# Performance work log

Hardware: AMD Instinct MI355X
Metric: run time of the kernel (lower is better)

## Reference

```python
import jax, jax.numpy as jnp
import numpy as np

N = 262144
H = 256
R = 32


def setup_inputs() -> dict:
    key = jax.random.key(0)
    ks = jax.random.split(key, 16)
    s = 1.0 / np.sqrt(H)
    return {
        "x": jax.random.normal(ks[0], (N, 1), jnp.float32),
        "t": jax.random.uniform(ks[1], (N, 1), jnp.float32),
        "start_w": jax.random.normal(ks[2], (H, 2), jnp.float32) * 0.5,
        "start_b": jax.random.normal(ks[3], (H,), jnp.float32) * 0.1,
        "end_w": jax.random.normal(ks[4], (1, H), jnp.float32) * s,
        "end_b": jax.random.normal(ks[5], (1,), jnp.float32) * 0.1,
        "col_0": jax.random.normal(ks[6], (H, R), jnp.float32) * s,
        "col_1": jax.random.normal(ks[7], (H, R), jnp.float32) * s,
        "col_2": jax.random.normal(ks[8], (H, R), jnp.float32) * s,
        "row_0": jax.random.normal(ks[9], (H, R), jnp.float32) * s,
        "row_1": jax.random.normal(ks[10], (H, R), jnp.float32) * s,
        "row_2": jax.random.normal(ks[11], (H, R), jnp.float32) * s,
        "alpha_0": jax.random.normal(ks[12], (R,), jnp.float32),
        "alpha_1": jax.random.normal(ks[13], (R,), jnp.float32),
        "alpha_2": jax.random.normal(ks[14], (R,), jnp.float32),
    }


def reference(x, t, start_w, start_b, end_w, end_b,
              col_0, col_1, col_2, row_0, row_1, row_2,
              alpha_0, alpha_1, alpha_2):
    # inputs: [N,2] -> start Linear -> tanh
    inp = jnp.concatenate([x, t], axis=1)
    h = jnp.tanh(inp @ start_w.T + start_b)  # [N, H]
    # three low-rank blocks: h @ (col * diag(alpha)) @ row.T, then tanh.
    # col_basis @ diag(alpha) == col_basis * alpha[None, :] (column scaling)
    for col, row, alpha in ((col_0, row_0, alpha_0),
                            (col_1, row_1, alpha_1),
                            (col_2, row_2, alpha_2)):
        h = jnp.tanh((h @ (col * alpha)) @ row.T)  # [N,H]->[N,R]->[N,H]
    return h @ end_w.T + end_b  # [N, 1]
```

## Files before the change

### kernel.cpp

```cpp
#include <hip/hip_runtime.h>


typedef _Float16 half4_t __attribute__((ext_vector_type(4)));
typedef __fp16   fp16x2  __attribute__((ext_vector_type(2)));
typedef float    float4_t __attribute__((ext_vector_type(4)));

#define TANH_SCALE 2.885390081777927f
#define MFMA16 __builtin_amdgcn_mfma_f32_16x16x16f16

namespace {

struct alignas(16) Smem {
  half4_t ctf[3 * 16 * 2 * 64];
  half4_t rwf[3 * 16 * 2 * 64];
  float w0[256], w1[256], bb[256];
  float ew[256];
  float rsC[3 * 32];
};

__device__ __forceinline__ half4_t pack4(float4_t v) {
  union { fp16x2 f2[2]; half4_t h4; } u;
  u.f2[0] = __builtin_amdgcn_cvt_pkrtz(v.x, v.y);
  u.f2[1] = __builtin_amdgcn_cvt_pkrtz(v.z, v.w);
  return u.h4;
}

__device__ __forceinline__ float inv_pre(float y) {
  return __builtin_amdgcn_rcpf(__builtin_amdgcn_exp2f(y) + 1.0f);
}

__device__ __forceinline__ half4_t inv4(float4_t v) {
  float4_t r;
  r.x = inv_pre(v.x); r.y = inv_pre(v.y);
  r.z = inv_pre(v.z); r.w = inv_pre(v.w);
  return pack4(r);
}

__global__ __launch_bounds__(1024)
__attribute__((amdgpu_waves_per_eu(4, 4)))
void pinn_fused(
    const float* __restrict__ xg, const float* __restrict__ tg,
    const float* __restrict__ sw, const float* __restrict__ sb,
    const float* __restrict__ ewp, const float* __restrict__ ebp,
    const float* __restrict__ c0, const float* __restrict__ c1,
    const float* __restrict__ c2, const float* __restrict__ r0,
    const float* __restrict__ r1, const float* __restrict__ r2,
    const float* __restrict__ a0, const float* __restrict__ a1,
    const float* __restrict__ a2, float* __restrict__ out, int n)
{
  __shared__ Smem sm;
  const int tid = threadIdx.x;

  for (int e = tid; e < 3 * 16 * 2 * 64; e += 1024) {
    const int lane_ = e & 63;
    const int sel   = (e >> 6) & 1;
    const int t_    = (e >> 7) & 15;
    const int k_    = e >> 11;
    const int m_ = lane_ & 15, q_ = lane_ >> 4;
    const float* ck = (k_ == 0) ? c0 : (k_ == 1) ? c1 : c2;
    const float* rk = (k_ == 0) ? r0 : (k_ == 1) ? r1 : r2;
    const float* ak = (k_ == 0) ? a0 : (k_ == 1) ? a1 : a2;
    {
      const int r = sel * 16 + m_;
      const float av = ak[r] * -2.0f;
      const int j0 = 16 * t_ + 4 * q_;
      half4_t v;
      v.x = (_Float16)(ck[(j0 + 0) * 32 + r] * av);
      v.y = (_Float16)(ck[(j0 + 1) * 32 + r] * av);
      v.z = (_Float16)(ck[(j0 + 2) * 32 + r] * av);
      v.w = (_Float16)(ck[(j0 + 3) * 32 + r] * av);
      sm.ctf[e] = v;
    }
    {
      const int j = 16 * t_ + m_;
      const int rr = sel * 16 + 4 * q_;
      half4_t v;
      v.x = (_Float16)(rk[j * 32 + rr + 0] * TANH_SCALE);
      v.y = (_Float16)(rk[j * 32 + rr + 1] * TANH_SCALE);
      v.z = (_Float16)(rk[j * 32 + rr + 2] * TANH_SCALE);
      v.w = (_Float16)(rk[j * 32 + rr + 3] * TANH_SCALE);
      sm.rwf[e] = v;
    }
  }
  if (tid < 256) {
    sm.w0[tid] = sw[2 * tid] * TANH_SCALE;
    sm.w1[tid] = sw[2 * tid + 1] * TANH_SCALE;
    sm.bb[tid] = sb[tid] * TANH_SCALE;
    sm.ew[tid] = ewp[tid] * -2.0f;
  }
  __syncthreads();

  if (tid < 96) {
    const int k_ = tid >> 5, r = tid & 31;
    const int sel = r >> 4, mm = r & 15;
    float s = 0.0f;
    for (int t = 0; t < 16; ++t)
      for (int qq = 0; qq < 4; ++qq) {
        const half4_t v = sm.ctf[((k_ * 16 + t) * 2 + sel) * 64 + 16 * qq + mm];
        s += (float)v.x + (float)v.y + (float)v.z + (float)v.w;
      }
    sm.rsC[k_ * 32 + r] = -0.5f * s;
  }
  __syncthreads();

  const int wave = tid >> 6;
  const int lane = tid & 63;
  const int m = lane & 15;
  const int q = lane >> 4;
  const int wo = 4 * q;
  const float ebv = ebp[0];
  const int tiles = n >> 4;

  float ewsum = 0.0f;
  for (int t = 0; t < 16; ++t) {
    const float4_t e4 = *(const float4_t*)&sm.ew[t * 16 + wo];
    ewsum += e4.x + e4.y + e4.z + e4.w;
  }
  ewsum *= -0.5f;

  const float4_t z4 = {0.f, 0.f, 0.f, 0.f};

#pragma unroll 1
  for (int g = (blockIdx.x * 16 + wave) * 4; g < tiles; g += 16384) {
    float xm[4], tm[4];
#pragma unroll
    for (int s = 0; s < 4; ++s) {
      xm[s] = xg[(g + s) * 16 + m];
      tm[s] = tg[(g + s) * 16 + m];
    }

    const float4_t rs00 = *(const float4_t*)&sm.rsC[wo];
    const float4_t rs01 = *(const float4_t*)&sm.rsC[16 + wo];
    float4_t acc[4][2];
#pragma unroll
    for (int s = 0; s < 4; ++s) { acc[s][0] = rs00; acc[s][1] = rs01; }
    const half4_t* cp0 = &sm.ctf[lane];
#pragma unroll 1
    for (int t = 0; t < 16; ++t) {
      const int cb = t * 16 + wo;
      const float4_t w0v = *(const float4_t*)&sm.w0[cb];
      const float4_t w1v = *(const float4_t*)&sm.w1[cb];
      const float4_t bv  = *(const float4_t*)&sm.bb[cb];
      half4_t h[4];
#pragma unroll
      for (int s = 0; s < 4; ++s) {
        float4_t z;
        z.x = fmaf(xm[s], w0v.x, fmaf(tm[s], w1v.x, bv.x));
        z.y = fmaf(xm[s], w0v.y, fmaf(tm[s], w1v.y, bv.y));
        z.z = fmaf(xm[s], w0v.z, fmaf(tm[s], w1v.z, bv.z));
        z.w = fmaf(xm[s], w0v.w, fmaf(tm[s], w1v.w, bv.w));
        h[s] = inv4(z);
      }
      const half4_t cA = cp0[0], cB = cp0[64];
#pragma unroll
      for (int s = 0; s < 4; ++s) acc[s][0] = MFMA16(cA, h[s], acc[s][0], 0, 0, 0);
#pragma unroll
      for (int s = 0; s < 4; ++s) acc[s][1] = MFMA16(cB, h[s], acc[s][1], 0, 0, 0);
      cp0 += 128;
    }

#pragma unroll 1
    for (int k = 0; k < 2; ++k) {
      half4_t pf[4][2];
#pragma unroll
      for (int s = 0; s < 4; ++s) {
        pf[s][0] = pack4(acc[s][0]);
        pf[s][1] = pack4(acc[s][1]);
      }
      const float4_t rsA = *(const float4_t*)&sm.rsC[(k + 1) * 32 + wo];
      const float4_t rsB = *(const float4_t*)&sm.rsC[(k + 1) * 32 + 16 + wo];
      float4_t nn[4][2];
#pragma unroll
      for (int s = 0; s < 4; ++s) { nn[s][0] = rsA; nn[s][1] = rsB; }
      const half4_t* rp = &sm.rwf[k * 2048 + lane];
      const half4_t* cp = &sm.ctf[(k + 1) * 2048 + lane];
#pragma unroll 1
      for (int t = 0; t < 16; ++t) {
        const half4_t rA = rp[0], rB = rp[64];
        const half4_t cA = cp[0], cB = cp[64];
        float4_t u[4];
#pragma unroll
        for (int s = 0; s < 4; ++s) u[s] = MFMA16(rA, pf[s][0], z4, 0, 0, 0);
#pragma unroll
        for (int s = 0; s < 4; ++s) u[s] = MFMA16(rB, pf[s][1], u[s], 0, 0, 0);
        half4_t h[4];
#pragma unroll
        for (int s = 0; s < 4; ++s) h[s] = inv4(u[s]);
#pragma unroll
        for (int s = 0; s < 4; ++s) nn[s][0] = MFMA16(cA, h[s], nn[s][0], 0, 0, 0);
#pragma unroll
        for (int s = 0; s < 4; ++s) nn[s][1] = MFMA16(cB, h[s], nn[s][1], 0, 0, 0);
        rp += 128; cp += 128;
      }
#pragma unroll
      for (int s = 0; s < 4; ++s) { acc[s][0] = nn[s][0]; acc[s][1] = nn[s][1]; }
    }

    float ssum[4] = {ewsum, ewsum, ewsum, ewsum};
    {
      half4_t pf[4][2];
#pragma unroll
      for (int s = 0; s < 4; ++s) {
        pf[s][0] = pack4(acc[s][0]);
        pf[s][1] = pack4(acc[s][1]);
      }
      const half4_t* rp = &sm.rwf[2 * 2048 + lane];
#pragma unroll 1
      for (int t = 0; t < 16; ++t) {
        const half4_t rA = rp[0], rB = rp[64];
        const float4_t ev = *(const float4_t*)&sm.ew[t * 16 + wo];
        float4_t u[4];
#pragma unroll
        for (int s = 0; s < 4; ++s) u[s] = MFMA16(rA, pf[s][0], z4, 0, 0, 0);
#pragma unroll
        for (int s = 0; s < 4; ++s) u[s] = MFMA16(rB, pf[s][1], u[s], 0, 0, 0);
#pragma unroll
        for (int s = 0; s < 4; ++s) {
          ssum[s] = fmaf(ev.x, inv_pre(u[s].x), ssum[s]);
          ssum[s] = fmaf(ev.y, inv_pre(u[s].y), ssum[s]);
          ssum[s] = fmaf(ev.z, inv_pre(u[s].z), ssum[s]);
          ssum[s] = fmaf(ev.w, inv_pre(u[s].w), ssum[s]);
        }
        rp += 128;
      }
    }

#pragma unroll
    for (int s = 0; s < 4; ++s) {
      ssum[s] += __shfl_xor(ssum[s], 16);
      ssum[s] += __shfl_xor(ssum[s], 32);
    }
    if (lane < 16) {
#pragma unroll
      for (int s = 0; s < 4; ++s) out[(g + s) * 16 + m] = ssum[s] + ebv;
    }
  }
}

}

extern "C" void kernel_launch(void* const* d_in, const int* in_sizes, int n_in,
                              void* d_out, int out_size, void* d_ws, size_t ws_size,
                              hipStream_t stream) {
  const float* xg  = (const float*)d_in[0];
  const float* tg  = (const float*)d_in[1];
  const float* sw  = (const float*)d_in[2];
  const float* sb  = (const float*)d_in[3];
  const float* ewp = (const float*)d_in[4];
  const float* ebp = (const float*)d_in[5];
  const float* c0  = (const float*)d_in[6];
  const float* c1  = (const float*)d_in[7];
  const float* c2  = (const float*)d_in[8];
  const float* r0  = (const float*)d_in[9];
  const float* r1  = (const float*)d_in[10];
  const float* r2  = (const float*)d_in[11];
  const float* a0  = (const float*)d_in[12];
  const float* a1  = (const float*)d_in[13];
  const float* a2  = (const float*)d_in[14];
  float* outp = (float*)d_out;

  const int n = in_sizes[0];

  pinn_fused<<<256, 1024, 0, stream>>>(xg, tg, sw, sb, ewp, ebp,
                                       c0, c1, c2, r0, r1, r2, a0, a1, a2,
                                       outp, n);
}
```

Measured before the change: 141.0 us.

## Move start-layer affine and end projection onto MFMA instructions

The per-element start-layer FMAs (x*w0 + t*w1 + b) become a 16x16x16 f16 MFMA. To keep input precision, x and t are split into hi/lo fp16 pairs, and the weights and bias are packed into a B fragment. The end-layer dot product with its cross-lane shuffle reduction also becomes an MFMA accumulation against an fp16-packed end-weight fragment, so each output lands directly in accumulator row 0. This moves VALU work onto the matrix cores but adds fp16 rounding of the start weights, bias and end weights, which may cost accuracy.

```diff
diff --git a/kernel.cpp b/kernel.cpp
--- a/kernel.cpp
+++ b/kernel.cpp
@@ -13,8 +13,8 @@
 struct alignas(16) Smem {
   half4_t ctf[3 * 16 * 2 * 64];
   half4_t rwf[3 * 16 * 2 * 64];
-  float w0[256], w1[256], bb[256];
-  float ew[256];
+  half4_t wff[16 * 64];
+  half4_t ewf[16 * 64];
   float rsC[3 * 32];
 };
 
@@ -82,11 +82,27 @@
       sm.rwf[e] = v;
     }
   }
-  if (tid < 256) {
-    sm.w0[tid] = sw[2 * tid] * TANH_SCALE;
-    sm.w1[tid] = sw[2 * tid + 1] * TANH_SCALE;
-    sm.bb[tid] = sb[tid] * TANH_SCALE;
-    sm.ew[tid] = ewp[tid] * -2.0f;
+  {
+    const int t_ = tid >> 6, lane_ = tid & 63;
+    const int m_ = lane_ & 15, q_ = lane_ >> 4;
+    const int j = 16 * t_ + m_;
+    half4_t v = {(_Float16)0.f, (_Float16)0.f, (_Float16)0.f, (_Float16)0.f};
+    if (q_ == 0) {
+      const float w0v = sw[2 * j] * TANH_SCALE;
+      const float w1v = sw[2 * j + 1] * TANH_SCALE;
+      v.x = (_Float16)w0v; v.y = (_Float16)w0v;
+      v.z = (_Float16)w1v; v.w = (_Float16)w1v;
+    } else if (q_ == 1) {
+      v.x = (_Float16)(sb[j] * TANH_SCALE);
+    }
+    sm.wff[tid] = v;
+    const int j0 = 16 * t_ + 4 * q_;
+    half4_t w;
+    w.x = (_Float16)(ewp[j0 + 0] * -2.0f);
+    w.y = (_Float16)(ewp[j0 + 1] * -2.0f);
+    w.z = (_Float16)(ewp[j0 + 2] * -2.0f);
+    w.w = (_Float16)(ewp[j0 + 3] * -2.0f);
+    sm.ewf[tid] = w;
   }
   __syncthreads();
 
@@ -111,22 +127,35 @@
   const float ebv = ebp[0];
   const int tiles = n >> 4;
 
-  float ewsum = 0.0f;
-  for (int t = 0; t < 16; ++t) {
-    const float4_t e4 = *(const float4_t*)&sm.ew[t * 16 + wo];
-    ewsum += e4.x + e4.y + e4.z + e4.w;
-  }
-  ewsum *= -0.5f;
+  float ewc;
+  {
+    float s = 0.0f;
+    for (int t = 0; t < 16; ++t) {
+      const half4_t e4 = sm.ewf[t * 64 + lane];
+      s += (float)e4.x + (float)e4.y + (float)e4.z + (float)e4.w;
+    }
+    s += __shfl_xor(s, 16);
+    s += __shfl_xor(s, 32);
+    ewc = -0.5f * s;
+  }
 
   const float4_t z4 = {0.f, 0.f, 0.f, 0.f};
 
 #pragma unroll 1
   for (int g = (blockIdx.x * 16 + wave) * 4; g < tiles; g += 16384) {
-    float xm[4], tm[4];
+    half4_t bs[4];
 #pragma unroll
     for (int s = 0; s < 4; ++s) {
-      xm[s] = xg[(g + s) * 16 + m];
-      tm[s] = tg[(g + s) * 16 + m];
+      const float xv = xg[(g + s) * 16 + m];
+      const float tv = tg[(g + s) * 16 + m];
+      const _Float16 xh = (_Float16)xv;
+      const _Float16 xl = (_Float16)(xv - (float)xh);
+      const _Float16 th = (_Float16)tv;
+      const _Float16 tl = (_Float16)(tv - (float)th);
+      const half4_t b0 = {xh, xl, th, tl};
+      const half4_t b1 = {(_Float16)1.0f, (_Float16)0.f, (_Float16)0.f, (_Float16)0.f};
+      const half4_t bz = {(_Float16)0.f, (_Float16)0.f, (_Float16)0.f, (_Float16)0.f};
+      bs[s] = (q == 0) ? b0 : ((q == 1) ? b1 : bz);
     }
 
     const float4_t rs00 = *(const float4_t*)&sm.rsC[wo];
@@ -134,29 +163,23 @@
     float4_t acc[4][2];
 #pragma unroll
     for (int s = 0; s < 4; ++s) { acc[s][0] = rs00; acc[s][1] = rs01; }
+    const half4_t* wp  = &sm.wff[lane];
     const half4_t* cp0 = &sm.ctf[lane];
 #pragma unroll 1
     for (int t = 0; t < 16; ++t) {
-      const int cb = t * 16 + wo;
-      const float4_t w0v = *(const float4_t*)&sm.w0[cb];
-      const float4_t w1v = *(const float4_t*)&sm.w1[cb];
-      const float4_t bv  = *(const float4_t*)&sm.bb[cb];
+      const half4_t wA = wp[0];
+      const half4_t cA = cp0[0], cB = cp0[64];
+      float4_t zz[4];
+#pragma unroll
+      for (int s = 0; s < 4; ++s) zz[s] = MFMA16(wA, bs[s], z4, 0, 0, 0);
       half4_t h[4];
 #pragma unroll
-      for (int s = 0; s < 4; ++s) {
-        float4_t z;
-        z.x = fmaf(xm[s], w0v.x, fmaf(tm[s], w1v.x, bv.x));
-        z.y = fmaf(xm[s], w0v.y, fmaf(tm[s], w1v.y, bv.y));
-        z.z = fmaf(xm[s], w0v.z, fmaf(tm[s], w1v.z, bv.z));
-        z.w = fmaf(xm[s], w0v.w, fmaf(tm[s], w1v.w, bv.w));
-        h[s] = inv4(z);
-      }
-      const half4_t cA = cp0[0], cB = cp0[64];
+      for (int s = 0; s < 4; ++s) h[s] = inv4(zz[s]);
 #pragma unroll
       for (int s = 0; s < 4; ++s) acc[s][0] = MFMA16(cA, h[s], acc[s][0], 0, 0, 0);
 #pragma unroll
       for (int s = 0; s < 4; ++s) acc[s][1] = MFMA16(cB, h[s], acc[s][1], 0, 0, 0);
-      cp0 += 128;
+      wp += 64; cp0 += 128;
     }
 
 #pragma unroll 1
@@ -196,7 +219,9 @@
       for (int s = 0; s < 4; ++s) { acc[s][0] = nn[s][0]; acc[s][1] = nn[s][1]; }
     }
 
-    float ssum[4] = {ewsum, ewsum, ewsum, ewsum};
+    float4_t ae[4];
+#pragma unroll
+    for (int s = 0; s < 4; ++s) ae[s] = z4;
     {
       half4_t pf[4][2];
 #pragma unroll
@@ -205,34 +230,28 @@
         pf[s][1] = pack4(acc[s][1]);
       }
       const half4_t* rp = &sm.rwf[2 * 2048 + lane];
+      const half4_t* ep = &sm.ewf[lane];
 #pragma unroll 1
       for (int t = 0; t < 16; ++t) {
         const half4_t rA = rp[0], rB = rp[64];
-        const float4_t ev = *(const float4_t*)&sm.ew[t * 16 + wo];
+        const half4_t eA = ep[0];
         float4_t u[4];
 #pragma unroll
         for (int s = 0; s < 4; ++s) u[s] = MFMA16(rA, pf[s][0], z4, 0, 0, 0);
 #pragma unroll
         for (int s = 0; s < 4; ++s) u[s] = MFMA16(rB, pf[s][1], u[s], 0, 0, 0);
-#pragma unroll
-        for (int s = 0; s < 4; ++s) {
-          ssum[s] = fmaf(ev.x, inv_pre(u[s].x), ssum[s]);
-          ssum[s] = fmaf(ev.y, inv_pre(u[s].y), ssum[s]);
-          ssum[s] = fmaf(ev.z, inv_pre(u[s].z), ssum[s]);
-          ssum[s] = fmaf(ev.w, inv_pre(u[s].w), ssum[s]);
-        }
-        rp += 128;
-      }
-    }
-
-#pragma unroll
-    for (int s = 0; s < 4; ++s) {
-      ssum[s] += __shfl_xor(ssum[s], 16);
-      ssum[s] += __shfl_xor(ssum[s], 32);
-    }
+        half4_t h[4];
+#pragma unroll
+        for (int s = 0; s < 4; ++s) h[s] = inv4(u[s]);
+#pragma unroll
+        for (int s = 0; s < 4; ++s) ae[s] = MFMA16(eA, h[s], ae[s], 0, 0, 0);
+        rp += 128; ep += 64;
+      }
+    }
+
     if (lane < 16) {
 #pragma unroll
-      for (int s = 0; s < 4; ++s) out[(g + s) * 16 + m] = ssum[s] + ebv;
+      for (int s = 0; s < 4; ++s) out[(g + s) * 16 + m] = ae[s].x + ewc + ebv;
     }
   }
 }
```

Measured after the change: 141.9 us. About the same (+0.7%).
